# Kernel tuning notes

Measured on AMD Instinct MI355X. Metric: run time of the kernel, lower is better.

## Reference

```python
import jax, jax.numpy as jnp
import numpy as np


def setup_inputs() -> dict:
    key = jax.random.key(0)
    k1, k2, k3 = jax.random.split(key, 3)
    B, D, H, W, K = 16, 512, 60, 60, 32
    std = 1.0 / np.sqrt(K * D)
    X = jax.random.normal(k1, (B, D, H, W), dtype=jnp.float32)
    codewords = jax.random.uniform(k2, (K, D), dtype=jnp.float32, minval=-std, maxval=std)
    # scale is drawn uniform(-1, 0) in the torch module (shake in train mode)
    scale = -jax.random.uniform(k3, (K,), dtype=jnp.float32)
    return {"X": X, "codewords": codewords, "scale": scale}


def reference(X, codewords, scale):
    # X: (B, D, H, W) -> flatten spatial to (B, N, D)
    B, D = X.shape[0], X.shape[1]
    Xf = X.reshape(B, D, -1).transpose(0, 2, 1)          # (B, N, D)
    # scaledL2: SL[b,n,k] = scale[k] * ||X[b,n] - C[k]||^2, expanded via GEMM
    # to avoid the (B, N, K, D) residual tensor.
    x2 = jnp.sum(Xf * Xf, axis=-1)                       # (B, N)
    c2 = jnp.sum(codewords * codewords, axis=-1)         # (K,)
    xc = jnp.einsum('bnd,kd->bnk', Xf, codewords)        # (B, N, K)
    sl = scale * (x2[..., None] - 2.0 * xc + c2)         # (B, N, K)
    A = jax.nn.softmax(sl, axis=2)                       # (B, N, K)
    # aggregate: E[b,k,d] = sum_n A[b,n,k] * (X[b,n,d] - C[k,d])
    E = jnp.einsum('bnk,bnd->bkd', A, Xf) - jnp.sum(A, axis=1)[..., None] * codewords
    return E                                             # (B, K, D)
```

## Files before the change

kernel.cpp:

```cpp
#include <hip/hip_runtime.h>
#include <hip/hip_bf16.h>

constexpr int BB = 16;
constexpr int DD = 512;
constexpr int NN = 3600;
constexpr int KK = 32;
constexpr int SB = 29;
constexpr int WIN = 128;

typedef __attribute__((ext_vector_type(8))) short short8;
typedef __attribute__((ext_vector_type(4))) float f32x4;

__device__ inline unsigned bf16pack(float a, float b) {
    unsigned ia = __float_as_uint(a), ib = __float_as_uint(b);
    ia = (ia + 0x7fffu + ((ia >> 16) & 1u)) >> 16;
    ib = (ib + 0x7fffu + ((ib >> 16) & 1u)) & 0xffff0000u;
    return ia | ib;
}

__global__ __launch_bounds__(256) void k0_prep(const float* __restrict__ Cw,
                                               const float* __restrict__ scale,
                                               ushort* __restrict__ Cbf,
                                               float* __restrict__ sc2) {
    __shared__ float buf[8][32];
    const int t = threadIdx.x;
    const int k = t & 31;
    const int h = t >> 5;
    const float4* row = reinterpret_cast<const float4*>(Cw + k * DD + h * 64);
    uint2* crow = reinterpret_cast<uint2*>(Cbf + k * DD + h * 64);
    float s = 0.f;
#pragma unroll
    for (int j = 0; j < 16; ++j) {
        float4 v = row[j];
        crow[j] = make_uint2(bf16pack(v.x, v.y), bf16pack(v.z, v.w));
        s += v.x * v.x + v.y * v.y + v.z * v.z + v.w * v.w;
    }
    buf[h][k] = s;
    __syncthreads();
    if (t < 32) {
        float tot = 0.f;
#pragma unroll
        for (int j = 0; j < 8; ++j) tot += buf[j][t];
        sc2[t] = scale[t] * tot;
    }
}

__global__ __launch_bounds__(512) void kf_fused(const float* __restrict__ X,
                                                const ushort* __restrict__ Cbf,
                                                const float* __restrict__ scale,
                                                const float* __restrict__ sc2,
                                                ushort* __restrict__ Epb,
                                                float* __restrict__ asum_part) {
    __shared__ ushort tile[DD * WIN];
    __shared__ ushort As2[KK * WIN];
    __shared__ float x2part[16][WIN];
    __shared__ float x2s[WIN];
    __shared__ float asw[8][KK];

    const int t = threadIdx.x;
    const int w = t >> 6;
    const int l = t & 63;
    const int q = l >> 4;
    const int r = l & 15;
    const int ng = t & 31;
    const int dgs = t >> 5;
    const int b = blockIdx.x / SB;
    const int sb = blockIdx.x % SB;
    const int n0 = sb * WIN;
    const float* Xb = X + (size_t)b * DD * NN;
    const ushort* cb0 = Cbf + r * DD + q * 8;
    const ushort* cb1 = cb0 + 16 * DD;

    int nst = n0 + ng * 4;
    if (nst > NN - 4) nst = NN - 4;
    const float* xsrc = Xb + nst;

    const int nloc = w * 16 + r;
    f32x4 a0 = {0.f, 0.f, 0.f, 0.f};
    f32x4 a1 = {0.f, 0.f, 0.f, 0.f};
    float x2loc[4] = {0.f, 0.f, 0.f, 0.f};

    float4 bufA[8], bufB[8];
#pragma unroll
    for (int i = 0; i < 8; ++i)
        bufA[i] = *reinterpret_cast<const float4*>(xsrc + (size_t)(dgs * 8 + i) * NN);

#define CHUNK_BODY(CURB, NXTB, C)                                              \
    {                                                                          \
        short8 cf0[4], cf1[4];                                                 \
        _Pragma("unroll")                                                      \
        for (int u = 0; u < 4; ++u) {                                          \
            cf0[u] = *reinterpret_cast<const short8*>(cb0 + ((C)*4 + u) * 32); \
            cf1[u] = *reinterpret_cast<const short8*>(cb1 + ((C)*4 + u) * 32); \
        }                                                                      \
        if ((C) < 3) {                                                         \
            _Pragma("unroll")                                                  \
            for (int i = 0; i < 8; ++i)                                        \
                NXTB[i] = *reinterpret_cast<const float4*>(                    \
                    xsrc + (size_t)(((C) + 1) * 128 + dgs * 8 + i) * NN);      \
        }                                                                      \
        _Pragma("unroll")                                                      \
        for (int i = 0; i < 8; ++i) {                                          \
            const float4 v = CURB[i];                                          \
            x2loc[0] = fmaf(v.x, v.x, x2loc[0]);                               \
            x2loc[1] = fmaf(v.y, v.y, x2loc[1]);                               \
            x2loc[2] = fmaf(v.z, v.z, x2loc[2]);                               \
            x2loc[3] = fmaf(v.w, v.w, x2loc[3]);                               \
            const int d = (C) * 128 + dgs * 8 + i;                             \
            *reinterpret_cast<uint2*>(                                         \
                &tile[d * WIN + ((ng * 4) ^ ((d & 7) << 3))]) =                \
                make_uint2(bf16pack(v.x, v.y), bf16pack(v.z, v.w));            \
        }                                                                      \
        asm volatile("s_waitcnt lgkmcnt(0)" ::: "memory");                     \
        __builtin_amdgcn_s_barrier();                                          \
        __builtin_amdgcn_sched_barrier(0);                                     \
        _Pragma("unroll")                                                      \
        for (int u = 0; u < 4; ++u) {                                          \
            const int s = (C) * 4 + u;                                         \
            union { short8 s8; ushort us[8]; } af;                             \
            _Pragma("unroll")                                                  \
            for (int jj = 0; jj < 8; ++jj)                                     \
                af.us[jj] = tile[(s * 32 + q * 8 + jj) * WIN + (nloc ^ (jj << 3))]; \
            a0 = __builtin_amdgcn_mfma_f32_16x16x32_bf16(af.s8, cf0[u], a0, 0, 0, 0); \
            a1 = __builtin_amdgcn_mfma_f32_16x16x32_bf16(af.s8, cf1[u], a1, 0, 0, 0); \
        }                                                                      \
    }

    CHUNK_BODY(bufA, bufB, 0)
    CHUNK_BODY(bufB, bufA, 1)
    CHUNK_BODY(bufA, bufB, 2)
    CHUNK_BODY(bufB, bufA, 3)
#undef CHUNK_BODY

    *reinterpret_cast<f32x4*>(&x2part[dgs][ng * 4]) =
        (f32x4){x2loc[0], x2loc[1], x2loc[2], x2loc[3]};
    __syncthreads();
    if (t < WIN) {
        float s = 0.f;
#pragma unroll
        for (int dg = 0; dg < 16; ++dg) s += x2part[dg][t];
        x2s[t] = s;
    }
    __syncthreads();

    const float sk0 = scale[r], sk1 = scale[r + 16];
    const float sq0 = sc2[r],  sq1 = sc2[r + 16];
    float e0v[4], e1v[4];
    float as0 = 0.f, as1 = 0.f;
#pragma unroll
    for (int i = 0; i < 4; ++i) {
        const float x2v = x2s[w * 16 + 4 * q + i];
        float sl0 = fmaf(sk0, x2v, sq0) - 2.f * sk0 * a0[i];
        float sl1 = fmaf(sk1, x2v, sq1) - 2.f * sk1 * a1[i];
        float m = fmaxf(sl0, sl1);
        m = fmaxf(m, __shfl_xor(m, 1));
        m = fmaxf(m, __shfl_xor(m, 2));
        m = fmaxf(m, __shfl_xor(m, 4));
        m = fmaxf(m, __shfl_xor(m, 8));
        float e0 = __expf(sl0 - m), e1 = __expf(sl1 - m);
        float ssum = e0 + e1;
        ssum += __shfl_xor(ssum, 1);
        ssum += __shfl_xor(ssum, 2);
        ssum += __shfl_xor(ssum, 4);
        ssum += __shfl_xor(ssum, 8);
        const float inv = 1.f / ssum;
        e0 *= inv; e1 *= inv;
        if (n0 + w * 16 + 4 * q + i >= NN) { e0 = 0.f; e1 = 0.f; }
        e0v[i] = e0; e1v[i] = e1;
        as0 += e0; as1 += e1;
    }
    *reinterpret_cast<uint2*>(&As2[r * WIN + ((w * 16 + 4 * q) ^ ((r & 7) << 3))]) =
        make_uint2(bf16pack(e0v[0], e0v[1]), bf16pack(e0v[2], e0v[3]));
    *reinterpret_cast<uint2*>(&As2[(r + 16) * WIN + ((w * 16 + 4 * q) ^ ((r & 7) << 3))]) =
        make_uint2(bf16pack(e1v[0], e1v[1]), bf16pack(e1v[2], e1v[3]));

    as0 += __shfl_xor(as0, 16); as0 += __shfl_xor(as0, 32);
    as1 += __shfl_xor(as1, 16); as1 += __shfl_xor(as1, 32);
    if (l < 16) { asw[w][r] = as0; asw[w][r + 16] = as1; }
    __syncthreads();
    if (t < KK) {
        float s = 0.f;
#pragma unroll
        for (int jw = 0; jw < 8; ++jw) s += asw[jw][t];
        asum_part[((size_t)b * SB + sb) * KK + t] = s;
    }

    short8 bfr0[4], bfr1[4];
#pragma unroll
    for (int step = 0; step < 4; ++step) {
        bfr0[step] = *reinterpret_cast<const short8*>(
            &As2[r * WIN + ((step * 32 + q * 8) ^ ((r & 7) << 3))]);
        bfr1[step] = *reinterpret_cast<const short8*>(
            &As2[(r + 16) * WIN + ((step * 32 + q * 8) ^ ((r & 7) << 3))]);
    }

    f32x4 acc[4][2];
#pragma unroll
    for (int df = 0; df < 4; ++df) {
        acc[df][0] = (f32x4){0.f, 0.f, 0.f, 0.f};
        acc[df][1] = (f32x4){0.f, 0.f, 0.f, 0.f};
    }

#pragma unroll
    for (int df = 0; df < 4; ++df) {
        const int d = w * 64 + df * 16 + r;
#pragma unroll
        for (int step = 0; step < 4; ++step) {
            const short8 xa = *reinterpret_cast<const short8*>(
                &tile[d * WIN + ((step * 32 + q * 8) ^ ((d & 7) << 3))]);
            acc[df][0] = __builtin_amdgcn_mfma_f32_16x16x32_bf16(
                xa, bfr0[step], acc[df][0], 0, 0, 0);
            acc[df][1] = __builtin_amdgcn_mfma_f32_16x16x32_bf16(
                xa, bfr1[step], acc[df][1], 0, 0, 0);
        }
    }

    ushort* ep = Epb + (size_t)(b * SB + sb) * KK * DD;
#pragma unroll
    for (int df = 0; df < 4; ++df) {
#pragma unroll
        for (int kf = 0; kf < 2; ++kf) {
            const int k = kf * 16 + r;
            const int d = w * 64 + df * 16 + q * 4;
            const f32x4 v = acc[df][kf];
            *reinterpret_cast<uint2*>(ep + (size_t)k * DD + d) =
                make_uint2(bf16pack(v[0], v[1]), bf16pack(v[2], v[3]));
        }
    }
}

__global__ __launch_bounds__(128) void k3_final(const ushort* __restrict__ Epb,
                                                const float* __restrict__ asum_part,
                                                const float* __restrict__ Cw,
                                                float* __restrict__ E) {
    const int t = threadIdx.x;
    const int b = blockIdx.x >> 5, k = blockIdx.x & 31;

    float asum = 0.f;
#pragma unroll
    for (int sb = 0; sb < SB; ++sb)
        asum += asum_part[((size_t)b * SB + sb) * KK + k];

    const int d = t * 4;
    float s0 = 0.f, s1 = 0.f, s2 = 0.f, s3 = 0.f;
    const ushort* base = Epb + ((size_t)b * SB * KK + k) * DD + d;
#pragma unroll 4
    for (int sb = 0; sb < SB; ++sb) {
        const uint2 u = *reinterpret_cast<const uint2*>(base + (size_t)sb * KK * DD);
        s0 += __uint_as_float(u.x << 16);
        s1 += __uint_as_float(u.x & 0xffff0000u);
        s2 += __uint_as_float(u.y << 16);
        s3 += __uint_as_float(u.y & 0xffff0000u);
    }
    const float4 c = *reinterpret_cast<const float4*>(Cw + k * DD + d);
    float4 o;
    o.x = s0 - asum * c.x;
    o.y = s1 - asum * c.y;
    o.z = s2 - asum * c.z;
    o.w = s3 - asum * c.w;
    *reinterpret_cast<float4*>(E + ((size_t)b * KK + k) * DD + d) = o;
}

extern "C" void kernel_launch(void* const* d_in, const int* in_sizes, int n_in,
                              void* d_out, int out_size, void* d_ws, size_t ws_size,
                              hipStream_t stream) {
    const float* X     = (const float*)d_in[0];
    const float* Cw    = (const float*)d_in[1];
    const float* scale = (const float*)d_in[2];
    float* E = (float*)d_out;

    float* ws = (float*)d_ws;
    ushort* Epb = (ushort*)ws;
    float* asum_part = ws + (size_t)BB * SB * KK * DD / 2;
    float* sc2 = asum_part + (size_t)BB * SB * KK;
    ushort* Cbf = (ushort*)(sc2 + KK);

    k0_prep<<<dim3(1), dim3(256), 0, stream>>>(Cw, scale, Cbf, sc2);
    kf_fused<<<dim3(BB * SB), dim3(512), 0, stream>>>(X, Cbf, scale, sc2, Epb, asum_part);
    k3_final<<<dim3(BB * KK), dim3(128), 0, stream>>>(Epb, asum_part, Cw, E);
}
```

Measured before the change: 52.60 us.

## Process two windows per block with cross-window prefetch of X

Each block of the fused kernel now handles two consecutive (batch, spatial-window) tiles instead of one, halving the grid to 232 blocks. During the last chunk of the first window it prefetches the first X chunk of the second window, so global loads overlap the softmax and aggregation phase. __syncthreads is replaced by an lgkmcnt wait plus a raw barrier. The risks are that a grid of 232 blocks may underfill the 256 CUs, and that the whole per-block path is serialized across the two windows.

```diff
diff --git a/kernel.cpp b/kernel.cpp
--- a/kernel.cpp
+++ b/kernel.cpp
@@ -7,6 +7,7 @@
 constexpr int KK = 32;
 constexpr int SB = 29;
 constexpr int WIN = 128;
+constexpr int PAIRS = 232;
 
 typedef __attribute__((ext_vector_type(8))) short short8;
 typedef __attribute__((ext_vector_type(4))) float f32x4;
@@ -17,6 +18,13 @@
     ib = (ib + 0x7fffu + ((ib >> 16) & 1u)) & 0xffff0000u;
     return ia | ib;
 }
+
+#define BARL()                                                        \
+    do {                                                              \
+        asm volatile("s_waitcnt lgkmcnt(0)" ::: "memory");            \
+        __builtin_amdgcn_s_barrier();                                 \
+        __builtin_amdgcn_sched_barrier(0);                            \
+    } while (0)
 
 __global__ __launch_bounds__(256) void k0_prep(const float* __restrict__ Cw,
                                                const float* __restrict__ scale,
@@ -64,26 +72,41 @@
     const int r = l & 15;
     const int ng = t & 31;
     const int dgs = t >> 5;
-    const int b = blockIdx.x / SB;
-    const int sb = blockIdx.x % SB;
-    const int n0 = sb * WIN;
-    const float* Xb = X + (size_t)b * DD * NN;
+
+    const int wg0 = blockIdx.x * 2;
+    const int wg1 = wg0 + 1;
+    const int b0 = wg0 / SB, sb0 = wg0 % SB;
+    const int b1 = wg1 / SB, sb1 = wg1 % SB;
+
+    auto make_xsrc = [&](int b, int sb) -> const float* {
+        int nst = sb * WIN + ng * 4;
+        if (nst > NN - 4) nst = NN - 4;
+        return X + (size_t)b * DD * NN + nst;
+    };
+    const float* xs0 = make_xsrc(b0, sb0);
+    const float* xs1 = make_xsrc(b1, sb1);
+
     const ushort* cb0 = Cbf + r * DD + q * 8;
     const ushort* cb1 = cb0 + 16 * DD;
-
-    int nst = n0 + ng * 4;
-    if (nst > NN - 4) nst = NN - 4;
-    const float* xsrc = Xb + nst;
-
     const int nloc = w * 16 + r;
-    f32x4 a0 = {0.f, 0.f, 0.f, 0.f};
-    f32x4 a1 = {0.f, 0.f, 0.f, 0.f};
-    float x2loc[4] = {0.f, 0.f, 0.f, 0.f};
+    const float sk0 = scale[r], sk1 = scale[r + 16];
+    const float sq0 = sc2[r],  sq1 = sc2[r + 16];
 
     float4 bufA[8], bufB[8];
-#pragma unroll
-    for (int i = 0; i < 8; ++i)
-        bufA[i] = *reinterpret_cast<const float4*>(xsrc + (size_t)(dgs * 8 + i) * NN);
+
+    auto window = [&](int b, int sb, const float* xsrc, const float* xsrc_next,
+                      bool skip_first, bool pf_next) {
+        const int n0 = sb * WIN;
+        f32x4 a0 = {0.f, 0.f, 0.f, 0.f};
+        f32x4 a1 = {0.f, 0.f, 0.f, 0.f};
+        float x2loc[4] = {0.f, 0.f, 0.f, 0.f};
+
+        if (!skip_first) {
+#pragma unroll
+            for (int i = 0; i < 8; ++i)
+                bufA[i] = *reinterpret_cast<const float4*>(
+                    xsrc + (size_t)(dgs * 8 + i) * NN);
+        }
 
 #define CHUNK_BODY(CURB, NXTB, C)                                              \
     {                                                                          \
@@ -98,6 +121,11 @@
             for (int i = 0; i < 8; ++i)                                        \
                 NXTB[i] = *reinterpret_cast<const float4*>(                    \
                     xsrc + (size_t)(((C) + 1) * 128 + dgs * 8 + i) * NN);      \
+        } else if (pf_next) {                                                  \
+            _Pragma("unroll")                                                  \
+            for (int i = 0; i < 8; ++i)                                        \
+                NXTB[i] = *reinterpret_cast<const float4*>(                    \
+                    xsrc_next + (size_t)(dgs * 8 + i) * NN);                   \
         }                                                                      \
         _Pragma("unroll")                                                      \
         for (int i = 0; i < 8; ++i) {                                          \
@@ -126,107 +154,110 @@
         }                                                                      \
     }
 
-    CHUNK_BODY(bufA, bufB, 0)
-    CHUNK_BODY(bufB, bufA, 1)
-    CHUNK_BODY(bufA, bufB, 2)
-    CHUNK_BODY(bufB, bufA, 3)
+        CHUNK_BODY(bufA, bufB, 0)
+        CHUNK_BODY(bufB, bufA, 1)
+        CHUNK_BODY(bufA, bufB, 2)
+        CHUNK_BODY(bufB, bufA, 3)
 #undef CHUNK_BODY
 
-    *reinterpret_cast<f32x4*>(&x2part[dgs][ng * 4]) =
-        (f32x4){x2loc[0], x2loc[1], x2loc[2], x2loc[3]};
-    __syncthreads();
-    if (t < WIN) {
-        float s = 0.f;
-#pragma unroll
-        for (int dg = 0; dg < 16; ++dg) s += x2part[dg][t];
-        x2s[t] = s;
-    }
-    __syncthreads();
-
-    const float sk0 = scale[r], sk1 = scale[r + 16];
-    const float sq0 = sc2[r],  sq1 = sc2[r + 16];
-    float e0v[4], e1v[4];
-    float as0 = 0.f, as1 = 0.f;
-#pragma unroll
-    for (int i = 0; i < 4; ++i) {
-        const float x2v = x2s[w * 16 + 4 * q + i];
-        float sl0 = fmaf(sk0, x2v, sq0) - 2.f * sk0 * a0[i];
-        float sl1 = fmaf(sk1, x2v, sq1) - 2.f * sk1 * a1[i];
-        float m = fmaxf(sl0, sl1);
-        m = fmaxf(m, __shfl_xor(m, 1));
-        m = fmaxf(m, __shfl_xor(m, 2));
-        m = fmaxf(m, __shfl_xor(m, 4));
-        m = fmaxf(m, __shfl_xor(m, 8));
-        float e0 = __expf(sl0 - m), e1 = __expf(sl1 - m);
-        float ssum = e0 + e1;
-        ssum += __shfl_xor(ssum, 1);
-        ssum += __shfl_xor(ssum, 2);
-        ssum += __shfl_xor(ssum, 4);
-        ssum += __shfl_xor(ssum, 8);
-        const float inv = 1.f / ssum;
-        e0 *= inv; e1 *= inv;
-        if (n0 + w * 16 + 4 * q + i >= NN) { e0 = 0.f; e1 = 0.f; }
-        e0v[i] = e0; e1v[i] = e1;
-        as0 += e0; as1 += e1;
-    }
-    *reinterpret_cast<uint2*>(&As2[r * WIN + ((w * 16 + 4 * q) ^ ((r & 7) << 3))]) =
-        make_uint2(bf16pack(e0v[0], e0v[1]), bf16pack(e0v[2], e0v[3]));
-    *reinterpret_cast<uint2*>(&As2[(r + 16) * WIN + ((w * 16 + 4 * q) ^ ((r & 7) << 3))]) =
-        make_uint2(bf16pack(e1v[0], e1v[1]), bf16pack(e1v[2], e1v[3]));
-
-    as0 += __shfl_xor(as0, 16); as0 += __shfl_xor(as0, 32);
-    as1 += __shfl_xor(as1, 16); as1 += __shfl_xor(as1, 32);
-    if (l < 16) { asw[w][r] = as0; asw[w][r + 16] = as1; }
-    __syncthreads();
-    if (t < KK) {
-        float s = 0.f;
-#pragma unroll
-        for (int jw = 0; jw < 8; ++jw) s += asw[jw][t];
-        asum_part[((size_t)b * SB + sb) * KK + t] = s;
-    }
-
-    short8 bfr0[4], bfr1[4];
-#pragma unroll
-    for (int step = 0; step < 4; ++step) {
-        bfr0[step] = *reinterpret_cast<const short8*>(
-            &As2[r * WIN + ((step * 32 + q * 8) ^ ((r & 7) << 3))]);
-        bfr1[step] = *reinterpret_cast<const short8*>(
-            &As2[(r + 16) * WIN + ((step * 32 + q * 8) ^ ((r & 7) << 3))]);
-    }
-
-    f32x4 acc[4][2];
-#pragma unroll
-    for (int df = 0; df < 4; ++df) {
-        acc[df][0] = (f32x4){0.f, 0.f, 0.f, 0.f};
-        acc[df][1] = (f32x4){0.f, 0.f, 0.f, 0.f};
-    }
-
-#pragma unroll
-    for (int df = 0; df < 4; ++df) {
-        const int d = w * 64 + df * 16 + r;
+        *reinterpret_cast<f32x4*>(&x2part[dgs][ng * 4]) =
+            (f32x4){x2loc[0], x2loc[1], x2loc[2], x2loc[3]};
+        BARL();
+        if (t < WIN) {
+            float s = 0.f;
+#pragma unroll
+            for (int dg = 0; dg < 16; ++dg) s += x2part[dg][t];
+            x2s[t] = s;
+        }
+        BARL();
+
+        float e0v[4], e1v[4];
+        float as0 = 0.f, as1 = 0.f;
+#pragma unroll
+        for (int i = 0; i < 4; ++i) {
+            const float x2v = x2s[w * 16 + 4 * q + i];
+            float sl0 = fmaf(sk0, x2v, sq0) - 2.f * sk0 * a0[i];
+            float sl1 = fmaf(sk1, x2v, sq1) - 2.f * sk1 * a1[i];
+            float m = fmaxf(sl0, sl1);
+            m = fmaxf(m, __shfl_xor(m, 1));
+            m = fmaxf(m, __shfl_xor(m, 2));
+            m = fmaxf(m, __shfl_xor(m, 4));
+            m = fmaxf(m, __shfl_xor(m, 8));
+            float e0 = __expf(sl0 - m), e1 = __expf(sl1 - m);
+            float ssum = e0 + e1;
+            ssum += __shfl_xor(ssum, 1);
+            ssum += __shfl_xor(ssum, 2);
+            ssum += __shfl_xor(ssum, 4);
+            ssum += __shfl_xor(ssum, 8);
+            const float inv = 1.f / ssum;
+            e0 *= inv; e1 *= inv;
+            if (n0 + w * 16 + 4 * q + i >= NN) { e0 = 0.f; e1 = 0.f; }
+            e0v[i] = e0; e1v[i] = e1;
+            as0 += e0; as1 += e1;
+        }
+        *reinterpret_cast<uint2*>(&As2[r * WIN + ((w * 16 + 4 * q) ^ ((r & 7) << 3))]) =
+            make_uint2(bf16pack(e0v[0], e0v[1]), bf16pack(e0v[2], e0v[3]));
+        *reinterpret_cast<uint2*>(&As2[(r + 16) * WIN + ((w * 16 + 4 * q) ^ ((r & 7) << 3))]) =
+            make_uint2(bf16pack(e1v[0], e1v[1]), bf16pack(e1v[2], e1v[3]));
+
+        as0 += __shfl_xor(as0, 16); as0 += __shfl_xor(as0, 32);
+        as1 += __shfl_xor(as1, 16); as1 += __shfl_xor(as1, 32);
+        if (l < 16) { asw[w][r] = as0; asw[w][r + 16] = as1; }
+        BARL();
+        if (t < KK) {
+            float s = 0.f;
+#pragma unroll
+            for (int jw = 0; jw < 8; ++jw) s += asw[jw][t];
+            asum_part[((size_t)b * SB + sb) * KK + t] = s;
+        }
+
+        short8 bfr0[4], bfr1[4];
 #pragma unroll
         for (int step = 0; step < 4; ++step) {
-            const short8 xa = *reinterpret_cast<const short8*>(
-                &tile[d * WIN + ((step * 32 + q * 8) ^ ((d & 7) << 3))]);
-            acc[df][0] = __builtin_amdgcn_mfma_f32_16x16x32_bf16(
-                xa, bfr0[step], acc[df][0], 0, 0, 0);
-            acc[df][1] = __builtin_amdgcn_mfma_f32_16x16x32_bf16(
-                xa, bfr1[step], acc[df][1], 0, 0, 0);
-        }
-    }
-
-    ushort* ep = Epb + (size_t)(b * SB + sb) * KK * DD;
-#pragma unroll
-    for (int df = 0; df < 4; ++df) {
-#pragma unroll
-        for (int kf = 0; kf < 2; ++kf) {
-            const int k = kf * 16 + r;
-            const int d = w * 64 + df * 16 + q * 4;
-            const f32x4 v = acc[df][kf];
-            *reinterpret_cast<uint2*>(ep + (size_t)k * DD + d) =
-                make_uint2(bf16pack(v[0], v[1]), bf16pack(v[2], v[3]));
-        }
-    }
+            bfr0[step] = *reinterpret_cast<const short8*>(
+                &As2[r * WIN + ((step * 32 + q * 8) ^ ((r & 7) << 3))]);
+            bfr1[step] = *reinterpret_cast<const short8*>(
+                &As2[(r + 16) * WIN + ((step * 32 + q * 8) ^ ((r & 7) << 3))]);
+        }
+
+        f32x4 acc[4][2];
+#pragma unroll
+        for (int df = 0; df < 4; ++df) {
+            acc[df][0] = (f32x4){0.f, 0.f, 0.f, 0.f};
+            acc[df][1] = (f32x4){0.f, 0.f, 0.f, 0.f};
+        }
+
+#pragma unroll
+        for (int df = 0; df < 4; ++df) {
+            const int d = w * 64 + df * 16 + r;
+#pragma unroll
+            for (int step = 0; step < 4; ++step) {
+                const short8 xa = *reinterpret_cast<const short8*>(
+                    &tile[d * WIN + ((step * 32 + q * 8) ^ ((d & 7) << 3))]);
+                acc[df][0] = __builtin_amdgcn_mfma_f32_16x16x32_bf16(
+                    xa, bfr0[step], acc[df][0], 0, 0, 0);
+                acc[df][1] = __builtin_amdgcn_mfma_f32_16x16x32_bf16(
+                    xa, bfr1[step], acc[df][1], 0, 0, 0);
+            }
+        }
+
+        ushort* ep = Epb + (size_t)(b * SB + sb) * KK * DD;
+#pragma unroll
+        for (int df = 0; df < 4; ++df) {
+#pragma unroll
+            for (int kf = 0; kf < 2; ++kf) {
+                const int k = kf * 16 + r;
+                const int d = w * 64 + df * 16 + q * 4;
+                const f32x4 v = acc[df][kf];
+                *reinterpret_cast<uint2*>(ep + (size_t)k * DD + d) =
+                    make_uint2(bf16pack(v[0], v[1]), bf16pack(v[2], v[3]));
+            }
+        }
+    };
+
+    window(b0, sb0, xs0, xs1, false, true);
+    BARL();
+    window(b1, sb1, xs1, nullptr, true, false);
 }
 
 __global__ __launch_bounds__(128) void k3_final(const ushort* __restrict__ Epb,
@@ -276,6 +307,6 @@
     ushort* Cbf = (ushort*)(sc2 + KK);
 
     k0_prep<<<dim3(1), dim3(256), 0, stream>>>(Cw, scale, Cbf, sc2);
-    kf_fused<<<dim3(BB * SB), dim3(512), 0, stream>>>(X, Cbf, scale, sc2, Epb, asum_part);
+    kf_fused<<<dim3(PAIRS), dim3(512), 0, stream>>>(X, Cbf, scale, sc2, Epb, asum_part);
     k3_final<<<dim3(BB * KK), dim3(128), 0, stream>>>(Epb, asum_part, Cw, E);
 }
```

Measured after the change: 77.36 us. +47.1%, slower.

## Parallelize codeword prep and stage partial E through LDS for coalesced stores

Applied to the files above, without the earlier changes.

The prep kernel now runs one block per codeword with a wavefront shuffle reduction instead of a single block doing all rows. In the fused kernel, per-block partial E results are written into the swizzled shared tile first and then stored to global memory with 16-byte coalesced writes. The partial buffer layout becomes (b,k,sb,d) so the final reduction reads contiguous rows. This adds two block barriers and reuses the X tile's LDS after it is no longer needed.

```diff
diff --git a/kernel.cpp b/kernel.cpp
--- a/kernel.cpp
+++ b/kernel.cpp
@@ -22,27 +22,17 @@
                                                const float* __restrict__ scale,
                                                ushort* __restrict__ Cbf,
                                                float* __restrict__ sc2) {
-    __shared__ float buf[8][32];
+    __shared__ float red[4];
+    const int k = blockIdx.x;
     const int t = threadIdx.x;
-    const int k = t & 31;
-    const int h = t >> 5;
-    const float4* row = reinterpret_cast<const float4*>(Cw + k * DD + h * 64);
-    uint2* crow = reinterpret_cast<uint2*>(Cbf + k * DD + h * 64);
-    float s = 0.f;
-#pragma unroll
-    for (int j = 0; j < 16; ++j) {
-        float4 v = row[j];
-        crow[j] = make_uint2(bf16pack(v.x, v.y), bf16pack(v.z, v.w));
-        s += v.x * v.x + v.y * v.y + v.z * v.z + v.w * v.w;
-    }
-    buf[h][k] = s;
-    __syncthreads();
-    if (t < 32) {
-        float tot = 0.f;
-#pragma unroll
-        for (int j = 0; j < 8; ++j) tot += buf[j][t];
-        sc2[t] = scale[t] * tot;
-    }
+    const float2 v = *reinterpret_cast<const float2*>(Cw + k * DD + t * 2);
+    *reinterpret_cast<unsigned*>(Cbf + k * DD + t * 2) = bf16pack(v.x, v.y);
+    float s = v.x * v.x + v.y * v.y;
+#pragma unroll
+    for (int o = 1; o < 64; o <<= 1) s += __shfl_xor(s, o);
+    if ((t & 63) == 0) red[t >> 6] = s;
+    __syncthreads();
+    if (t == 0) sc2[k] = scale[k] * (red[0] + red[1] + red[2] + red[3]);
 }
 
 __global__ __launch_bounds__(512) void kf_fused(const float* __restrict__ X,
@@ -215,7 +205,7 @@
         }
     }
 
-    ushort* ep = Epb + (size_t)(b * SB + sb) * KK * DD;
+    __syncthreads();
 #pragma unroll
     for (int df = 0; df < 4; ++df) {
 #pragma unroll
@@ -223,8 +213,21 @@
             const int k = kf * 16 + r;
             const int d = w * 64 + df * 16 + q * 4;
             const f32x4 v = acc[df][kf];
-            *reinterpret_cast<uint2*>(ep + (size_t)k * DD + d) =
+            *reinterpret_cast<uint2*>(&tile[k * DD + (d ^ ((k & 7) << 3))]) =
                 make_uint2(bf16pack(v[0], v[1]), bf16pack(v[2], v[3]));
+        }
+    }
+    __syncthreads();
+    {
+        ushort* ep = Epb + (((size_t)b * KK) * SB + sb) * DD;
+#pragma unroll
+        for (int p = 0; p < 4; ++p) {
+            const int g = p * 512 + t;
+            const int k = g >> 6;
+            const int gc = g & 63;
+            const uint4 vv = *reinterpret_cast<const uint4*>(
+                &tile[k * DD + ((gc * 8) ^ ((k & 7) << 3))]);
+            *reinterpret_cast<uint4*>(ep + (size_t)k * SB * DD + gc * 8) = vv;
         }
     }
 }
@@ -243,10 +246,10 @@
 
     const int d = t * 4;
     float s0 = 0.f, s1 = 0.f, s2 = 0.f, s3 = 0.f;
-    const ushort* base = Epb + ((size_t)b * SB * KK + k) * DD + d;
+    const ushort* base = Epb + ((size_t)(b * KK + k)) * SB * DD + d;
 #pragma unroll 4
     for (int sb = 0; sb < SB; ++sb) {
-        const uint2 u = *reinterpret_cast<const uint2*>(base + (size_t)sb * KK * DD);
+        const uint2 u = *reinterpret_cast<const uint2*>(base + (size_t)sb * DD);
         s0 += __uint_as_float(u.x << 16);
         s1 += __uint_as_float(u.x & 0xffff0000u);
         s2 += __uint_as_float(u.y << 16);
@@ -275,7 +278,7 @@
     float* sc2 = asum_part + (size_t)BB * SB * KK;
     ushort* Cbf = (ushort*)(sc2 + KK);
 
-    k0_prep<<<dim3(1), dim3(256), 0, stream>>>(Cw, scale, Cbf, sc2);
+    k0_prep<<<dim3(KK), dim3(256), 0, stream>>>(Cw, scale, Cbf, sc2);
     kf_fused<<<dim3(BB * SB), dim3(512), 0, stream>>>(X, Cbf, scale, sc2, Epb, asum_part);
     k3_final<<<dim3(BB * KK), dim3(128), 0, stream>>>(Epb, asum_part, Cw, E);
 }
```

New measurement: 50.06 us. 4.8% less time.
